# Kernel tuning notes

Hardware: AMD Instinct MI355X
Metric: run time of the kernel (lower is better)

The kernel has to match this reference:

```python
import jax, jax.numpy as jnp
import numpy as np

V, E, H2, T = 50000, 256, 512, 16  # vocab, embed, hidden_dim, tagset
H = H2 // 2                        # per-direction hidden
START, STOP = 14, 15
NEG = -10000.0


def setup_inputs() -> dict:
    key = jax.random.key(0)
    ks = jax.random.split(key, 13)
    s = 0.08
    tokens = jax.random.randint(ks[0], (32, 512), 0, V)
    embed_table = jax.random.normal(ks[1], (V, E), jnp.float32)
    Wi_f = jax.random.normal(ks[2], (4 * H, E), jnp.float32) * s
    Wh_f = jax.random.normal(ks[3], (4 * H, H), jnp.float32) * s
    bi_f = jnp.zeros((4 * H,), jnp.float32)
    bh_f = jnp.zeros((4 * H,), jnp.float32)
    Wi_b = jax.random.normal(ks[4], (4 * H, E), jnp.float32) * s
    Wh_b = jax.random.normal(ks[5], (4 * H, H), jnp.float32) * s
    bi_b = jnp.zeros((4 * H,), jnp.float32)
    bh_b = jnp.zeros((4 * H,), jnp.float32)
    Wt = jax.random.normal(ks[6], (T, H2), jnp.float32) * s
    bt = jnp.zeros((T,), jnp.float32)
    trans = jax.random.normal(ks[7], (T, T), jnp.float32)
    trans = trans.at[START, :].set(NEG).at[:, STOP].set(NEG)
    return {"tokens": tokens, "embed_table": embed_table,
            "Wi_f": Wi_f, "Wh_f": Wh_f, "bi_f": bi_f, "bh_f": bh_f,
            "Wi_b": Wi_b, "Wh_b": Wh_b, "bi_b": bi_b, "bh_b": bh_b,
            "Wt": Wt, "bt": bt, "transitions": trans}


def _lstm_dir(x, Wi, Wh, bi, bh, reverse=False):
    # x: [S, B, E] -> h seq [S, B, H], PyTorch gate order i,f,g,o
    S, B, _ = x.shape
    xs = x[::-1] if reverse else x
    pre = jnp.einsum('sbe,ge->sbg', xs, Wi) + bi + bh  # precompute input GEMM

    def step(carry, z_t):
        h, c = carry
        z = z_t + h @ Wh.T  # [B, 4H]
        i, f, g, o = jnp.split(z, 4, axis=-1)
        c = jax.nn.sigmoid(f) * c + jax.nn.sigmoid(i) * jnp.tanh(g)
        h = jax.nn.sigmoid(o) * jnp.tanh(c)
        return (h, c), h

    h0 = jnp.zeros((B, H), x.dtype)
    _, hs = jax.lax.scan(step, (h0, h0), pre)
    return hs[::-1] if reverse else hs


def reference(tokens, embed_table, Wi_f, Wh_f, bi_f, bh_f,
              Wi_b, Wh_b, bi_b, bh_b, Wt, bt, transitions):
    x = embed_table[tokens]                # [B, S, E]
    x = jnp.transpose(x, (1, 0, 2))        # [S, B, E] seq-first like nn.LSTM
    hf = _lstm_dir(x, Wi_f, Wh_f, bi_f, bh_f, reverse=False)
    hb = _lstm_dir(x, Wi_b, Wh_b, bi_b, bh_b, reverse=True)
    feats = jnp.concatenate([hf, hb], axis=-1)           # [S, B, 2H]
    emissions = jnp.einsum('sbh,th->sbt', feats, Wt) + bt  # [S, B, T]

    B = tokens.shape[0]
    alpha0 = jnp.full((B, T), NEG, jnp.float32).at[:, START].set(0.0)

    def crf_step(alpha, emit_t):
        # alpha: [B, T_prev]; transitions[next, prev]; emit_t: [B, T_next]
        scores = alpha[:, None, :] + transitions[None, :, :] + emit_t[:, :, None]
        return jax.nn.logsumexp(scores, axis=2), None

    alpha, _ = jax.lax.scan(crf_step, alpha0, emissions)
    log_Z = jax.nn.logsumexp(alpha + transitions[STOP][None, :], axis=1)  # [B]
    return log_Z
```

## Files before the change

kernel.cpp:

```cpp
#include <hip/hip_runtime.h>
#include <hip/hip_bf16.h>
#include <stdint.h>

typedef __attribute__((ext_vector_type(4))) float f32x4;
typedef __attribute__((ext_vector_type(8))) short bf16x8;

#define SENT 0xFFFFFFFFFFFFFFFFULL

#define WS_XBF   0u
#define WS_WIR   8388608u
#define WS_BIAS  9437184u
#define WS_PRE   9445376u
#define WS_HALL  76554240u
#define WS_CTL   93364224u
#define WS_EMIS  93368320u
#define WS_CHK   94416896u

__device__ __forceinline__ unsigned short f2bf(float x) {
    union { float f; unsigned int u; } v; v.f = x;
    return (unsigned short)((v.u + 0x7FFFu + ((v.u >> 16) & 1u)) >> 16);
}
__device__ __forceinline__ float bf2f(unsigned short b) {
    union { float f; unsigned int u; } v; v.u = ((unsigned int)b) << 16; return v.f;
}
__device__ __forceinline__ unsigned int pack2(float a, float b) {
    return (unsigned int)f2bf(a) | ((unsigned int)f2bf(b) << 16);
}
__device__ __forceinline__ float sigf(float x)  { return 1.0f / (1.0f + __expf(-x)); }
__device__ __forceinline__ float tanhf_(float x){ return 1.0f - 2.0f / (__expf(2.0f * x) + 1.0f); }

__device__ __forceinline__ void lds_barrier() {
    asm volatile("s_waitcnt lgkmcnt(0)" ::: "memory");
    __builtin_amdgcn_s_barrier();
    __builtin_amdgcn_sched_barrier(0);
}

__global__ __launch_bounds__(256) void k_prep(
    const int* __restrict__ tokens, const float* __restrict__ embed,
    const float* __restrict__ Wi_f, const float* __restrict__ Wi_b,
    const float* __restrict__ bi_f, const float* __restrict__ bh_f,
    const float* __restrict__ bi_b, const float* __restrict__ bh_b,
    char* __restrict__ ws)
{
    int blk = blockIdx.x, tid = threadIdx.x;
    unsigned short* xbf  = (unsigned short*)(ws + WS_XBF);
    unsigned short* wir  = (unsigned short*)(ws + WS_WIR);
    float* biasr         = (float*)(ws + WS_BIAS);
    if (blk < 2048) {
        int rr = tid >> 5, cc = tid & 31;
        int r = blk * 8 + rr;
        int s = r >> 5, b = r & 31;
        int tok = tokens[b * 512 + s];
        int k = cc * 8;
        const float* src = embed + (size_t)tok * 256 + k;
        float4 a = *(const float4*)src;
        float4 c = *(const float4*)(src + 4);
        uint4 o; o.x = pack2(a.x, a.y); o.y = pack2(a.z, a.w);
        o.z = pack2(c.x, c.y); o.w = pack2(c.z, c.w);
        *(uint4*)(xbf + (size_t)r * 256 + k) = o;
    } else if (blk < 2304) {
        int rr = tid >> 5, cc = tid & 31;
        int rowp = (blk - 2048) * 8 + rr;
        int dir = rowp >> 10, q = rowp & 1023;
        int j = q >> 8, rs = q & 255;
        int g = rs >> 6, hl = rs & 63;
        int srow = g * 256 + j * 64 + hl;
        const float* W = dir ? Wi_b : Wi_f;
        int k = cc * 8;
        const float* src = W + (size_t)srow * 256 + k;
        float4 a = *(const float4*)src;
        float4 c = *(const float4*)(src + 4);
        uint4 o; o.x = pack2(a.x, a.y); o.y = pack2(a.z, a.w);
        o.z = pack2(c.x, c.y); o.w = pack2(c.z, c.w);
        *(uint4*)(wir + (size_t)rowp * 256 + k) = o;
        if (cc == 0)
            biasr[rowp] = dir ? (bi_b[srow] + bh_b[srow]) : (bi_f[srow] + bh_f[srow]);
    } else {
        if (blk == 2304 && tid < 16)
            ((unsigned int*)(ws + WS_CTL))[tid] = 0u;
        size_t g = (size_t)(blk - 2304) * 256 + tid;
        uint4* hall4 = (uint4*)(ws + WS_HALL);
        const unsigned int NF = 0xFFFFFFFFu;
        for (size_t u = g; u < 1050624u; u += 65536u) {
            size_t slot = (u >> 10) % 513u;
            uint4 val;
            if (slot == 0) { val.x = 0u; val.y = 0u; val.z = 0u; val.w = 0u; }
            else           { val.x = NF; val.y = NF; val.z = NF; val.w = NF; }
            hall4[u] = val;
        }
    }
}

__global__ __launch_bounds__(256) void k_pregemm(char* __restrict__ ws)
{
    __shared__ unsigned short Asb[128 * 136];
    __shared__ unsigned short Bsb[64 * 136];
    const unsigned short* xbf = (const unsigned short*)(ws + WS_XBF);
    const unsigned short* wir = (const unsigned short*)(ws + WS_WIR);
    const float* biasr        = (const float*)(ws + WS_BIAS);
    unsigned short* pre       = (unsigned short*)(ws + WS_PRE);
    int blk = blockIdx.x, tid = threadIdx.x;
    int mb = blk >> 5, nb = blk & 31;
    int Mbase = mb * 128, Nbase = nb * 64;
    int w = tid >> 6, l = tid & 63, col = l & 15, quad = l >> 4;
    f32x4 acc[4][2];
    #pragma unroll
    for (int a = 0; a < 4; ++a)
        #pragma unroll
        for (int b = 0; b < 2; ++b) acc[a][b] = (f32x4){0.f, 0.f, 0.f, 0.f};

    for (int kh = 0; kh < 2; ++kh) {
        __syncthreads();
        #pragma unroll
        for (int i = 0; i < 8; ++i) {
            int c = tid + i * 256;
            int row = c >> 4, c16 = c & 15;
            uint4 v = *(const uint4*)(xbf + ((size_t)(Mbase + row) * 256 + kh * 128 + c16 * 8));
            *(uint4*)(Asb + row * 136 + c16 * 8) = v;
        }
        #pragma unroll
        for (int i = 0; i < 4; ++i) {
            int c = tid + i * 256;
            int row = c >> 4, c16 = c & 15;
            uint4 v = *(const uint4*)(wir + ((size_t)(Nbase + row) * 256 + kh * 128 + c16 * 8));
            *(uint4*)(Bsb + row * 136 + c16 * 8) = v;
        }
        __syncthreads();
        int mhalf = w >> 1, nh = w & 1;
        #pragma unroll
        for (int kt = 0; kt < 4; ++kt) {
            bf16x8 bfr[2];
            #pragma unroll
            for (int nn = 0; nn < 2; ++nn)
                bfr[nn] = *(const bf16x8*)(Bsb + (16 * (nh * 2 + nn) + col) * 136 + kt * 32 + quad * 8);
            #pragma unroll
            for (int mm = 0; mm < 4; ++mm) {
                bf16x8 afr = *(const bf16x8*)(Asb + (16 * (mhalf * 4 + mm) + col) * 136 + kt * 32 + quad * 8);
                #pragma unroll
                for (int nn = 0; nn < 2; ++nn)
                    acc[mm][nn] = __builtin_amdgcn_mfma_f32_16x16x32_bf16(afr, bfr[nn], acc[mm][nn], 0, 0, 0);
            }
        }
    }
    #pragma unroll
    for (int mm = 0; mm < 4; ++mm) {
        int m_t = (w >> 1) * 4 + mm;
        int s = (Mbase >> 5) + (m_t >> 1);
        int bhalf = m_t & 1;
        #pragma unroll
        for (int nn = 0; nn < 2; ++nn) {
            int ncol = Nbase + 16 * ((w & 1) * 2 + nn) + col;
            int dir = ncol >> 10, j = (ncol >> 8) & 3, r = ncol & 255;
            int g = r >> 6, hl16 = (r >> 4) & 3;
            int tidp = (bhalf * 4 + hl16) * 64 + l;
            float bv = biasr[ncol];
            f32x4 a = acc[mm][nn];
            uint2 o;
            o.x = pack2(a[0] + bv, a[1] + bv);
            o.y = pack2(a[2] + bv, a[3] + bv);
            size_t off = (((size_t)(dir * 512 + s) * 4 + j) * 512 + tidp) * 16 + g * 4;
            *(uint2*)(pre + off) = o;
        }
    }
}

__global__ __launch_bounds__(512, 2) void k_rec(
    const float* __restrict__ Wh_f, const float* __restrict__ Wh_b, char* __restrict__ ws)
{
    __shared__ unsigned short hbuf[32 * 264];
    __shared__ unsigned short hst[8 * 16 * 20];
    __shared__ char stpad[71680];
    __shared__ int sRole;
    int tid = threadIdx.x;

    if (tid == 0) {
        ((volatile char*)stpad)[0] = 0;
        int xcd;
        asm volatile("s_getreg_b32 %0, hwreg(HW_REG_XCC_ID)" : "=s"(xcd));
        xcd &= 7;
        unsigned int* ctl = (unsigned int*)(ws + WS_CTL);
        unsigned int slot = __hip_atomic_fetch_add(&ctl[xcd], 1u,
                              __ATOMIC_RELAXED, __HIP_MEMORY_SCOPE_AGENT);
        int role = -1;
        if (slot < 8u) {
            if (slot == 7u) {
                unsigned int expv = 0u;
                __hip_atomic_compare_exchange_strong(&ctl[8], &expv, (unsigned int)(xcd + 1),
                    __ATOMIC_RELAXED, __ATOMIC_RELAXED, __HIP_MEMORY_SCOPE_AGENT);
            }
            unsigned int ts; long gc = 0;
            do {
                ts = __hip_atomic_fetch_add(&ctl[8], 0u,
                        __ATOMIC_RELAXED, __HIP_MEMORY_SCOPE_AGENT);
            } while (ts == 0u && ++gc < (1L << 26));
            if (ts == (unsigned int)(xcd + 1)) role = (int)slot;
        }
        sRole = role;
    }
    __syncthreads();
    int role = sRole;
    if (role < 0) return;
    int dir = role >> 2, j = role & 3;

    int w = tid >> 6, l = tid & 63, col = l & 15, quad = l >> 4;
    int m = w >> 2, hl16 = w & 3;
    const float* Wh = dir ? Wh_b : Wh_f;
    const unsigned short* pre = (const unsigned short*)(ws + WS_PRE);
    unsigned short* hall      = (unsigned short*)(ws + WS_HALL);

    bf16x8 wf[4][8];
    #pragma unroll
    for (int g = 0; g < 4; ++g) {
        int grow = g * 256 + j * 64 + hl16 * 16 + col;
        #pragma unroll
        for (int kt = 0; kt < 8; ++kt) {
            const float* src = Wh + (size_t)grow * 256 + kt * 32 + quad * 8;
            float4 x0 = *(const float4*)src;
            float4 x1 = *(const float4*)(src + 4);
            bf16x8 f;
            f[0] = (short)f2bf(x0.x); f[1] = (short)f2bf(x0.y);
            f[2] = (short)f2bf(x0.z); f[3] = (short)f2bf(x0.w);
            f[4] = (short)f2bf(x1.x); f[5] = (short)f2bf(x1.y);
            f[6] = (short)f2bf(x1.z); f[7] = (short)f2bf(x1.w);
            wf[g][kt] = f;
        }
    }
    for (int u = tid; u < 1280; u += 512) ((unsigned int*)hst)[u] = 0;
    __syncthreads();

    float cst[4] = {0.f, 0.f, 0.f, 0.f};
    size_t hbase_u = (size_t)dir * 513 * 8192;
    int row0 = tid >> 6, c8 = tid & 63;
    bool ownl = (c8 >= j * 16) && (c8 < j * 16 + 16);

    uint4 pn0, pn1;
    {
        int s0 = dir ? 511 : 0;
        const uint4* pp = (const uint4*)(pre + ((((size_t)(dir * 512 + s0)) * 4 + j) * 512 + tid) * 16);
        pn0 = pp[0]; pn1 = pp[1];
    }

    for (int st = 0; st < 512; ++st) {
        uint4 p0 = pn0, p1 = pn1;
        {
            int stn = (st < 511) ? st + 1 : st;
            int sn = dir ? (511 - stn) : stn;
            const uint4* pp = (const uint4*)(pre + ((((size_t)(dir * 512 + sn)) * 4 + j) * 512 + tid) * 16);
            pn0 = pp[0]; pn1 = pp[1];
        }

        unsigned short* hsl = hall + hbase_u + (size_t)st * 8192;
        unsigned long long v[4];
        if (ownl) {
            int lc = c8 * 4 - j * 64;
            int hl = lc >> 4, c4 = lc & 15;
            #pragma unroll
            for (int i = 0; i < 4; ++i) {
                int row = row0 + i * 8;
                int wp = (row >> 4) * 4 + hl, r_in = row & 15;
                v[i] = *(const unsigned long long*)(hst + wp * 320 + r_in * 20 + c4);
            }
        } else {
            #pragma unroll
            for (int i = 0; i < 4; ++i) {
                unsigned long long expv = SENT;
                __hip_atomic_compare_exchange_strong(
                    (unsigned long long*)(hsl + (size_t)(tid + i * 512) * 4), &expv, SENT,
                    __ATOMIC_RELAXED, __ATOMIC_RELAXED, __HIP_MEMORY_SCOPE_WORKGROUP);
                v[i] = expv;
            }
            bool pend = (v[0] == SENT) | (v[1] == SENT) | (v[2] == SENT) | (v[3] == SENT);
            int rnd = 0;
            while (pend && rnd < (1 << 20)) {
                #pragma unroll
                for (int i = 0; i < 4; ++i) {
                    if (v[i] == SENT) {
                        unsigned long long expv = SENT;
                        __hip_atomic_compare_exchange_strong(
                            (unsigned long long*)(hsl + (size_t)(tid + i * 512) * 4), &expv, SENT,
                            __ATOMIC_RELAXED, __ATOMIC_RELAXED, __HIP_MEMORY_SCOPE_WORKGROUP);
                        v[i] = expv;
                    }
                }
                pend = (v[0] == SENT) | (v[1] == SENT) | (v[2] == SENT) | (v[3] == SENT);
                ++rnd;
            }
        }
        #pragma unroll
        for (int i = 0; i < 4; ++i)
            *(unsigned long long*)(hbuf + (row0 + i * 8) * 264 + c8 * 4) = v[i];
        lds_barrier();

        f32x4 acc[4];
        #pragma unroll
        for (int g = 0; g < 4; ++g) acc[g] = (f32x4){0.f, 0.f, 0.f, 0.f};
        #pragma unroll
        for (int kt = 0; kt < 8; ++kt) {
            bf16x8 af = *(const bf16x8*)(hbuf + (m * 16 + col) * 264 + kt * 32 + quad * 8);
            #pragma unroll
            for (int g = 0; g < 4; ++g)
                acc[g] = __builtin_amdgcn_mfma_f32_16x16x32_bf16(af, wf[g][kt], acc[g], 0, 0, 0);
        }
        unsigned int pw[8] = {p0.x, p0.y, p0.z, p0.w, p1.x, p1.y, p1.z, p1.w};
        float z[4][4];
        #pragma unroll
        for (int g = 0; g < 4; ++g) {
            #pragma unroll
            for (int r2 = 0; r2 < 2; ++r2) {
                unsigned int u = pw[g * 2 + r2];
                z[g][r2 * 2]     = acc[g][r2 * 2]     + bf2f((unsigned short)(u & 0xffff));
                z[g][r2 * 2 + 1] = acc[g][r2 * 2 + 1] + bf2f((unsigned short)(u >> 16));
            }
        }
        unsigned short hb16[4];
        #pragma unroll
        for (int r = 0; r < 4; ++r) {
            float ci = sigf(z[1][r]) * cst[r] + sigf(z[0][r]) * tanhf_(z[2][r]);
            cst[r] = ci;
            hb16[r] = f2bf(sigf(z[3][r]) * tanhf_(ci));
        }
        unsigned short* hw = hst + w * 320;
        #pragma unroll
        for (int r = 0; r < 4; ++r) hw[(quad * 4 + r) * 20 + col] = hb16[r];
        int rrow = l >> 2, cpart = l & 3;
        unsigned long long hv = *(const unsigned long long*)(hw + rrow * 20 + cpart * 4);
        size_t dsto = hbase_u + (size_t)(st + 1) * 8192 + (size_t)(m * 16 + rrow) * 256
                    + j * 64 + hl16 * 16 + cpart * 4;
        (void)__hip_atomic_exchange((unsigned long long*)(hall + dsto), hv,
                                    __ATOMIC_RELAXED, __HIP_MEMORY_SCOPE_WORKGROUP);
        lds_barrier();
    }
}

__global__ __launch_bounds__(256) void k_emis(
    const float* __restrict__ Wt, const float* __restrict__ bt, char* __restrict__ ws)
{
    __shared__ float WtL[16 * 528];
    __shared__ unsigned short hrow[16 * 536];
    __shared__ float btL[16];
    int blk = blockIdx.x, tid = threadIdx.x;
    int sbb = blk * 16;
    int s = sbb >> 5, bbase = sbb & 31;
    const unsigned short* hall = (const unsigned short*)(ws + WS_HALL);
    float* emis = (float*)(ws + WS_EMIS);
    #pragma unroll
    for (int i = 0; i < 8; ++i) {
        int c = tid + i * 256;
        int trow = c >> 7, c128 = c & 127;
        float4 v = *(const float4*)(Wt + (size_t)trow * 512 + c128 * 4);
        *(float4*)(WtL + trow * 528 + c128 * 4) = v;
    }
    #pragma unroll
    for (int i = 0; i < 4; ++i) {
        int c = tid + i * 256;
        int row = c >> 6, c6 = c & 63, half = c6 >> 5, c16 = c6 & 31;
        size_t base = half == 0 ? (size_t)(s + 1) * 8192 : ((size_t)513 + (512 - s)) * 8192;
        uint4 v = *(const uint4*)(hall + base + (size_t)(bbase + row) * 256 + c16 * 8);
        *(uint4*)(hrow + row * 536 + half * 256 + c16 * 8) = v;
    }
    if (tid < 16) btL[tid] = bt[tid];
    __syncthreads();
    int t = tid >> 4, i = tid & 15;
    float acc = btL[t];
    const float* wrow = WtL + t * 528;
    const unsigned short* hr = hrow + i * 536;
    #pragma unroll 8
    for (int k = 0; k < 512; k += 4) {
        uint2 hu = *(const uint2*)(hr + k);
        float4 wv = *(const float4*)(wrow + k);
        acc += bf2f((unsigned short)(hu.x & 0xffff)) * wv.x
             + bf2f((unsigned short)(hu.x >> 16))    * wv.y
             + bf2f((unsigned short)(hu.y & 0xffff)) * wv.z
             + bf2f((unsigned short)(hu.y >> 16))    * wv.w;
    }
    emis[((size_t)(bbase + i) * 512 + s) * 16 + t] = acc;
}

__global__ __launch_bounds__(256) void k_crfc(const float* __restrict__ trans, char* __restrict__ ws)
{
    __shared__ float trL[16 * 17];
    __shared__ float est[16 * 16];
    __shared__ float Pb[2][16 * 17];
    int blk = blockIdx.x, tid = threadIdx.x;
    int b = blk >> 5, c = blk & 31;
    int t = tid >> 4, p = tid & 15;
    const float* emis = (const float*)(ws + WS_EMIS);
    float* chk = (float*)(ws + WS_CHK);
    trL[t * 17 + p] = trans[t * 16 + p];
    est[t * 16 + p] = emis[((size_t)b * 512 + c * 16 + t) * 16 + p];
    __syncthreads();
    float tr[16];
    #pragma unroll
    for (int q = 0; q < 16; ++q) tr[q] = trL[t * 17 + q];
    float out = trL[t * 17 + p] + est[0 * 16 + t];
    Pb[0][t * 17 + p] = out;
    __syncthreads();
    int cur = 0;
    for (int si = 1; si < 16; ++si) {
        float v[16]; float mx = -3.0e38f;
        #pragma unroll
        for (int q = 0; q < 16; ++q) { v[q] = tr[q] + Pb[cur][q * 17 + p]; mx = fmaxf(mx, v[q]); }
        float ss = 0.f;
        #pragma unroll
        for (int q = 0; q < 16; ++q) ss += __expf(v[q] - mx);
        out = est[si * 16 + t] + mx + __logf(ss);
        Pb[1 - cur][t * 17 + p] = out;
        __syncthreads();
        cur = 1 - cur;
    }
    chk[(size_t)(b * 32 + c) * 256 + t * 16 + p] = out;
}

__global__ __launch_bounds__(256) void k_crff(
    const float* __restrict__ trans, char* __restrict__ ws, float* __restrict__ out)
{
    __shared__ float Cst[16 * 17];
    __shared__ float Pb[2][16 * 17];
    __shared__ float af[16];
    int b = blockIdx.x, tid = threadIdx.x;
    int t = tid >> 4, p = tid & 15;
    const float* chk = (const float*)(ws + WS_CHK);
    Pb[0][t * 17 + p] = chk[(size_t)(b * 32) * 256 + t * 16 + p];
    __syncthreads();
    int cur = 0;
    for (int ci = 1; ci < 32; ++ci) {
        Cst[t * 17 + p] = chk[(size_t)(b * 32 + ci) * 256 + t * 16 + p];
        __syncthreads();
        float v[16]; float mx = -3.0e38f;
        #pragma unroll
        for (int q = 0; q < 16; ++q) { v[q] = Cst[t * 17 + q] + Pb[cur][q * 17 + p]; mx = fmaxf(mx, v[q]); }
        float ss = 0.f;
        #pragma unroll
        for (int q = 0; q < 16; ++q) ss += __expf(v[q] - mx);
        float outv = mx + __logf(ss);
        Pb[1 - cur][t * 17 + p] = outv;
        __syncthreads();
        cur = 1 - cur;
    }
    float vfin = Pb[cur][t * 17 + p] + ((p == 14) ? 0.0f : -10000.0f);
    Cst[t * 17 + p] = vfin;
    __syncthreads();
    if (tid < 16) {
        float mx = -3.0e38f;
        for (int q = 0; q < 16; ++q) mx = fmaxf(mx, Cst[tid * 17 + q]);
        float ss = 0.f;
        for (int q = 0; q < 16; ++q) ss += __expf(Cst[tid * 17 + q] - mx);
        af[tid] = mx + __logf(ss) + trans[15 * 16 + tid];
    }
    __syncthreads();
    if (tid == 0) {
        float mx = -3.0e38f;
        for (int q = 0; q < 16; ++q) mx = fmaxf(mx, af[q]);
        float ss = 0.f;
        for (int q = 0; q < 16; ++q) ss += __expf(af[q] - mx);
        out[b] = mx + __logf(ss);
    }
}

extern "C" void kernel_launch(void* const* d_in, const int* in_sizes, int n_in,
                              void* d_out, int out_size, void* d_ws, size_t ws_size,
                              hipStream_t stream)
{
    const int*   tokens = (const int*)d_in[0];
    const float* embed  = (const float*)d_in[1];
    const float* Wi_f   = (const float*)d_in[2];
    const float* Wh_f   = (const float*)d_in[3];
    const float* bi_f   = (const float*)d_in[4];
    const float* bh_f   = (const float*)d_in[5];
    const float* Wi_b   = (const float*)d_in[6];
    const float* Wh_b   = (const float*)d_in[7];
    const float* bi_b   = (const float*)d_in[8];
    const float* bh_b   = (const float*)d_in[9];
    const float* Wt     = (const float*)d_in[10];
    const float* bt     = (const float*)d_in[11];
    const float* trans  = (const float*)d_in[12];
    char* ws = (char*)d_ws;
    float* out = (float*)d_out;

    hipLaunchKernelGGL(k_prep, dim3(2560), dim3(256), 0, stream,
                       tokens, embed, Wi_f, Wi_b, bi_f, bh_f, bi_b, bh_b, ws);
    hipLaunchKernelGGL(k_pregemm, dim3(4096), dim3(256), 0, stream, ws);
    hipLaunchKernelGGL(k_rec, dim3(128), dim3(512), 0, stream, Wh_f, Wh_b, ws);
    hipLaunchKernelGGL(k_emis, dim3(1024), dim3(256), 0, stream, Wt, bt, ws);
    hipLaunchKernelGGL(k_crfc, dim3(1024), dim3(256), 0, stream, trans, ws);
    hipLaunchKernelGGL(k_crff, dim3(32), dim3(256), 0, stream, trans, ws, out);
}
```

Baseline: 1.619 ms.

## Replace per-element sentinel polling with per-step flag signalling between recurrence blocks

```diff
diff --git a/kernel.cpp b/kernel.cpp
--- a/kernel.cpp
+++ b/kernel.cpp
@@ -4,8 +4,6 @@
 
 typedef __attribute__((ext_vector_type(4))) float f32x4;
 typedef __attribute__((ext_vector_type(8))) short bf16x8;
-
-#define SENT 0xFFFFFFFFFFFFFFFFULL
 
 #define WS_XBF   0u
 #define WS_WIR   8388608u
@@ -15,6 +13,7 @@
 #define WS_CTL   93364224u
 #define WS_EMIS  93368320u
 #define WS_CHK   94416896u
+#define WS_FLG   WS_CHK
 
 __device__ __forceinline__ unsigned short f2bf(float x) {
     union { float f; unsigned int u; } v; v.f = x;
@@ -78,6 +77,10 @@
     } else {
         if (blk == 2304 && tid < 16)
             ((unsigned int*)(ws + WS_CTL))[tid] = 0u;
+        if (blk == 2305) {
+            unsigned int* flg = (unsigned int*)(ws + WS_FLG);
+            for (int u = tid; u < 2 * 513 * 4 * 32; u += 256) flg[u] = 0u;
+        }
         size_t g = (size_t)(blk - 2304) * 256 + tid;
         uint4* hall4 = (uint4*)(ws + WS_HALL);
         const unsigned int NF = 0xFFFFFFFFu;
@@ -168,13 +171,14 @@
     const float* __restrict__ Wh_f, const float* __restrict__ Wh_b, char* __restrict__ ws)
 {
     __shared__ unsigned short hbuf[32 * 264];
-    __shared__ unsigned short hst[8 * 16 * 20];
     __shared__ char stpad[71680];
     __shared__ int sRole;
+    __shared__ int goCnt;
     int tid = threadIdx.x;
 
     if (tid == 0) {
         ((volatile char*)stpad)[0] = 0;
+        goCnt = 0;
         int xcd;
         asm volatile("s_getreg_b32 %0, hwreg(HW_REG_XCC_ID)" : "=s"(xcd));
         xcd &= 7;
@@ -207,6 +211,7 @@
     const float* Wh = dir ? Wh_b : Wh_f;
     const unsigned short* pre = (const unsigned short*)(ws + WS_PRE);
     unsigned short* hall      = (unsigned short*)(ws + WS_HALL);
+    unsigned int* flags       = (unsigned int*)(ws + WS_FLG);
 
     bf16x8 wf[4][8];
     #pragma unroll
@@ -225,13 +230,12 @@
             wf[g][kt] = f;
         }
     }
-    for (int u = tid; u < 1280; u += 512) ((unsigned int*)hst)[u] = 0;
     __syncthreads();
 
     float cst[4] = {0.f, 0.f, 0.f, 0.f};
     size_t hbase_u = (size_t)dir * 513 * 8192;
     int row0 = tid >> 6, c8 = tid & 63;
-    bool ownl = (c8 >= j * 16) && (c8 < j * 16 + 16);
+    int jr = (tid < 3) ? (tid + (tid >= j ? 1 : 0)) : -1;
 
     uint4 pn0, pn1;
     {
@@ -242,50 +246,33 @@
 
     for (int st = 0; st < 512; ++st) {
         uint4 p0 = pn0, p1 = pn1;
-        {
-            int stn = (st < 511) ? st + 1 : st;
-            int sn = dir ? (511 - stn) : stn;
-            const uint4* pp = (const uint4*)(pre + ((((size_t)(dir * 512 + sn)) * 4 + j) * 512 + tid) * 16);
-            pn0 = pp[0]; pn1 = pp[1];
-        }
-
-        unsigned short* hsl = hall + hbase_u + (size_t)st * 8192;
+
+        if (st > 0) {
+            if (jr >= 0) {
+                unsigned int* fl = flags + ((size_t)((dir * 513 + st) * 4 + jr)) * 32;
+                int rnd = 0;
+                for (;;) {
+                    unsigned int expv = 0u;
+                    __hip_atomic_compare_exchange_strong(fl, &expv, 0u,
+                        __ATOMIC_RELAXED, __ATOMIC_RELAXED, __HIP_MEMORY_SCOPE_WORKGROUP);
+                    if (expv != 0u) break;
+                    if (++rnd > (1 << 18)) break;
+                }
+                __hip_atomic_fetch_add(&goCnt, 1, __ATOMIC_RELAXED, __HIP_MEMORY_SCOPE_WORKGROUP);
+            }
+            int target = 3 * st;
+            long sg = 0;
+            while (__hip_atomic_load(&goCnt, __ATOMIC_RELAXED, __HIP_MEMORY_SCOPE_WORKGROUP) < target) {
+                if (++sg > (1L << 21)) break;
+            }
+            asm volatile("" ::: "memory");
+        }
+
+        const unsigned short* hsl = hall + hbase_u + (size_t)st * 8192;
         unsigned long long v[4];
-        if (ownl) {
-            int lc = c8 * 4 - j * 64;
-            int hl = lc >> 4, c4 = lc & 15;
-            #pragma unroll
-            for (int i = 0; i < 4; ++i) {
-                int row = row0 + i * 8;
-                int wp = (row >> 4) * 4 + hl, r_in = row & 15;
-                v[i] = *(const unsigned long long*)(hst + wp * 320 + r_in * 20 + c4);
-            }
-        } else {
-            #pragma unroll
-            for (int i = 0; i < 4; ++i) {
-                unsigned long long expv = SENT;
-                __hip_atomic_compare_exchange_strong(
-                    (unsigned long long*)(hsl + (size_t)(tid + i * 512) * 4), &expv, SENT,
-                    __ATOMIC_RELAXED, __ATOMIC_RELAXED, __HIP_MEMORY_SCOPE_WORKGROUP);
-                v[i] = expv;
-            }
-            bool pend = (v[0] == SENT) | (v[1] == SENT) | (v[2] == SENT) | (v[3] == SENT);
-            int rnd = 0;
-            while (pend && rnd < (1 << 20)) {
-                #pragma unroll
-                for (int i = 0; i < 4; ++i) {
-                    if (v[i] == SENT) {
-                        unsigned long long expv = SENT;
-                        __hip_atomic_compare_exchange_strong(
-                            (unsigned long long*)(hsl + (size_t)(tid + i * 512) * 4), &expv, SENT,
-                            __ATOMIC_RELAXED, __ATOMIC_RELAXED, __HIP_MEMORY_SCOPE_WORKGROUP);
-                        v[i] = expv;
-                    }
-                }
-                pend = (v[0] == SENT) | (v[1] == SENT) | (v[2] == SENT) | (v[3] == SENT);
-                ++rnd;
-            }
-        }
+        #pragma unroll
+        for (int i = 0; i < 4; ++i)
+            v[i] = *(const unsigned long long*)(hsl + (size_t)(tid + i * 512) * 4);
         #pragma unroll
         for (int i = 0; i < 4; ++i)
             *(unsigned long long*)(hbuf + (row0 + i * 8) * 264 + c8 * 4) = v[i];
@@ -319,16 +306,23 @@
             cst[r] = ci;
             hb16[r] = f2bf(sigf(z[3][r]) * tanhf_(ci));
         }
-        unsigned short* hw = hst + w * 320;
-        #pragma unroll
-        for (int r = 0; r < 4; ++r) hw[(quad * 4 + r) * 20 + col] = hb16[r];
-        int rrow = l >> 2, cpart = l & 3;
-        unsigned long long hv = *(const unsigned long long*)(hw + rrow * 20 + cpart * 4);
-        size_t dsto = hbase_u + (size_t)(st + 1) * 8192 + (size_t)(m * 16 + rrow) * 256
-                    + j * 64 + hl16 * 16 + cpart * 4;
-        (void)__hip_atomic_exchange((unsigned long long*)(hall + dsto), hv,
-                                    __ATOMIC_RELAXED, __HIP_MEMORY_SCOPE_WORKGROUP);
-        lds_barrier();
+        size_t dstb = hbase_u + (size_t)(st + 1) * 8192
+                    + (size_t)(m * 16 + quad * 4) * 256 + j * 64 + hl16 * 16 + col;
+        #pragma unroll
+        for (int r = 0; r < 4; ++r)
+            *(hall + dstb + (size_t)r * 256) = hb16[r];
+        asm volatile("s_waitcnt vmcnt(0)" ::: "memory");
+        __builtin_amdgcn_s_barrier();
+        __builtin_amdgcn_sched_barrier(0);
+        if (tid == 0)
+            (void)__hip_atomic_exchange(flags + ((size_t)((dir * 513 + st + 1) * 4 + j)) * 32, 1u,
+                                        __ATOMIC_RELAXED, __HIP_MEMORY_SCOPE_WORKGROUP);
+        {
+            int stn = (st < 511) ? st + 1 : st;
+            int sn = dir ? (511 - stn) : stn;
+            const uint4* pp = (const uint4*)(pre + ((((size_t)(dir * 512 + sn)) * 4 + j) * 512 + tid) * 16);
+            pn0 = pp[0]; pn1 = pp[1];
+        }
     }
 }
 
```

Result: slower. 1.724 ms (+6.5%).
